# Kernel optimization log

Measured on AMD Instinct MI355X. Metric: run time of the kernel, lower is better.

## Reference

```python
import jax, jax.numpy as jnp
import numpy as np

B, T, S = 2, 1024, 1024
D_Q, D_KV, D_OUT = 2048, 2048, 2048
N_Q, N_KV, H = 16, 4, 128
G = N_Q // N_KV  # GQA groups
MIN_TS, MAX_TS = 1.0, 10000.0
SDPA_SCALE = 1.0  # dia uses scale=1.0 in F.scaled_dot_product_attention


def setup_inputs() -> dict:
    key = jax.random.key(0)
    ks = jax.random.split(key, 6)
    Xq = jax.random.normal(ks[0], (B, T, D_Q), jnp.float32)
    Xkv = jax.random.normal(ks[1], (B, S, D_KV), jnp.float32)
    q_positions = jnp.broadcast_to(jnp.arange(T, dtype=jnp.int32), (B, T))
    kv_positions = jnp.broadcast_to(jnp.arange(S, dtype=jnp.int32), (B, S))
    Wq = jax.random.normal(ks[2], (D_Q, N_Q, H), jnp.float32) * (D_Q ** -0.5)
    Wk = jax.random.normal(ks[3], (D_KV, N_KV, H), jnp.float32) * (D_KV ** -0.5)
    Wv = jax.random.normal(ks[4], (D_KV, N_KV, H), jnp.float32) * (D_KV ** -0.5)
    Wo = jax.random.normal(ks[5], (N_Q, H, D_OUT), jnp.float32) * ((N_Q * H) ** -0.5)
    return {"Xq": Xq, "Xkv": Xkv, "q_positions": q_positions,
            "kv_positions": kv_positions, "Wq": Wq, "Wk": Wk, "Wv": Wv, "Wo": Wo}


def _apply_rope(x, positions):
    # x: (B, L, N, H); positions: (B, L) int
    half = H // 2
    fraction = 2.0 * jnp.arange(half, dtype=jnp.float32) / H
    timescale = MIN_TS * (MAX_TS / MIN_TS) ** fraction  # (half,)
    sinusoid = positions.astype(jnp.float32)[:, :, None, None] / timescale  # (B,L,1,half)
    sin, cos = jnp.sin(sinusoid), jnp.cos(sinusoid)
    x = x.astype(jnp.float32)
    x1, x2 = jnp.split(x, 2, axis=-1)
    return jnp.concatenate([x1 * cos - x2 * sin, x2 * cos + x1 * sin], axis=-1)


def reference(Xq, Xkv, q_positions, kv_positions, Wq, Wk, Wv, Wo):
    # QKV projections (DenseGeneral): (B,L,D) x (D,N,H) -> (B,L,N,H)
    q = jnp.einsum('btd,dnh->btnh', Xq, Wq)
    k = jnp.einsum('bsd,dnh->bsnh', Xkv, Wk)
    v = jnp.einsum('bsd,dnh->bsnh', Xkv, Wv)
    # RoPE on q and k
    q = _apply_rope(q, q_positions)
    k = _apply_rope(k, kv_positions)
    # GQA attention, scale = 1.0 (as in dia), no mask, non-causal
    q = q.transpose(0, 2, 1, 3).reshape(B, N_KV, G, T, H)  # (B,K,G,T,H)
    k = k.transpose(0, 2, 1, 3)                             # (B,K,S,H)
    v = v.transpose(0, 2, 1, 3)                             # (B,K,S,H)
    scores = jnp.einsum('bkgth,bksh->bkgts', q, k) * SDPA_SCALE
    probs = jax.nn.softmax(scores, axis=-1)
    attn = jnp.einsum('bkgts,bksh->bkgth', probs, v)        # (B,K,G,T,H)
    attn = attn.reshape(B, N_Q, T, H).transpose(0, 2, 1, 3)  # (B,T,N,H)
    # Output projection (DenseGeneral contracting (N,H))
    out = jnp.einsum('btnh,nho->bto', attn, Wo)
    return out
```

## Files before the change

kernel.cpp:

```cpp
#include <hip/hip_runtime.h>
#include <hip/hip_bf16.h>
#include <math.h>
#include <stdint.h>

#define B_SZ 2
#define T_SZ 1024
#define S_SZ 1024
#define NQ 16
#define NKV 4
#define HD 128
#define DQ 2048
#define DKV 2048
#define DOUT 2048

typedef _Float16 half8 __attribute__((ext_vector_type(8)));
typedef _Float16 half4 __attribute__((ext_vector_type(4)));
typedef float f32x4 __attribute__((ext_vector_type(4)));

__device__ __forceinline__ half8 load8_f16(const _Float16* p) {
    return *reinterpret_cast<const half8*>(p);
}

__device__ __forceinline__ void stage16(const _Float16* g, _Float16* l, int lane) {
#if __has_builtin(__builtin_amdgcn_global_load_lds)
    __builtin_amdgcn_global_load_lds(
        (const __attribute__((address_space(1))) uint32_t*)g,
        (__attribute__((address_space(3))) uint32_t*)l, 16, 0, 0);
#else
    *reinterpret_cast<half8*>(l + lane * 8) = *reinterpret_cast<const half8*>(g);
#endif
}

__device__ __forceinline__ void conv_blk(const float* __restrict__ in,
                                         _Float16* __restrict__ out, int vb) {
    size_t i = ((size_t)vb * 256 + threadIdx.x) * 8;
    float4 a = *reinterpret_cast<const float4*>(in + i);
    float4 b = *reinterpret_cast<const float4*>(in + i + 4);
    half8 r;
    r[0] = (_Float16)a.x; r[1] = (_Float16)a.y; r[2] = (_Float16)a.z; r[3] = (_Float16)a.w;
    r[4] = (_Float16)b.x; r[5] = (_Float16)b.y; r[6] = (_Float16)b.z; r[7] = (_Float16)b.w;
    *reinterpret_cast<half8*>(out + i) = r;
}

__device__ __forceinline__ void tr_blk(const float* __restrict__ in,
                                       _Float16* __restrict__ out,
                                       int R, int C, int bx, int by,
                                       _Float16 (*tile)[72]) {
    const int tx = threadIdx.x & 15, ty = threadIdx.x >> 4;
    const int r0 = by * 64, c0 = bx * 64;
    #pragma unroll
    for (int i = 0; i < 4; ++i) {
        int r = ty + i * 16;
        float4 v = *reinterpret_cast<const float4*>(&in[(size_t)(r0 + r) * C + c0 + tx * 4]);
        tile[r][tx * 4 + 0] = (_Float16)v.x;
        tile[r][tx * 4 + 1] = (_Float16)v.y;
        tile[r][tx * 4 + 2] = (_Float16)v.z;
        tile[r][tx * 4 + 3] = (_Float16)v.w;
    }
    __syncthreads();
    #pragma unroll
    for (int i = 0; i < 4; ++i) {
        int oc = ty + i * 16;
        half4 v;
        v[0] = tile[tx * 4 + 0][oc];
        v[1] = tile[tx * 4 + 1][oc];
        v[2] = tile[tx * 4 + 2][oc];
        v[3] = tile[tx * 4 + 3][oc];
        *reinterpret_cast<half4*>(&out[(size_t)(c0 + oc) * R + r0 + tx * 4]) = v;
    }
}

__device__ __forceinline__ void tr16_blk(const _Float16* __restrict__ in,
                                         _Float16* __restrict__ out,
                                         int Cin, int Cout, int r0, int c0,
                                         _Float16 (*tile)[72]) {
    const int tx = threadIdx.x & 15, ty = threadIdx.x >> 4;
    #pragma unroll
    for (int i = 0; i < 4; ++i) {
        int r = ty + i * 16;
        half4 v = *reinterpret_cast<const half4*>(&in[(size_t)(r0 + r) * Cin + c0 + tx * 4]);
        tile[r][tx * 4 + 0] = v[0];
        tile[r][tx * 4 + 1] = v[1];
        tile[r][tx * 4 + 2] = v[2];
        tile[r][tx * 4 + 3] = v[3];
    }
    __syncthreads();
    #pragma unroll
    for (int i = 0; i < 4; ++i) {
        int oc = ty + i * 16;
        half4 v;
        v[0] = tile[tx * 4 + 0][oc];
        v[1] = tile[tx * 4 + 1][oc];
        v[2] = tile[tx * 4 + 2][oc];
        v[3] = tile[tx * 4 + 3][oc];
        *reinterpret_cast<half4*>(&out[(size_t)(c0 + oc) * Cout + r0 + tx * 4]) = v;
    }
}

__device__ __forceinline__ void rope_blk(_Float16* __restrict__ x,
                                         const int* __restrict__ pos,
                                         int N, int rowStride, int vb) {
    size_t idx = (size_t)vb * 256 + threadIdx.x;
    int h = (int)(idx & 63);
    size_t g = idx >> 6;
    int n = (int)(g % (size_t)N);
    size_t bl = g / (size_t)N;
    float p = (float)pos[bl];
    float ts = powf(10000.f, (float)h * (1.f / 64.f));
    float ang = p / ts;
    float s = sinf(ang), c = cosf(ang);
    size_t base = bl * (size_t)rowStride + (size_t)n * HD;
    float x1 = (float)x[base + h];
    float x2 = (float)x[base + h + 64];
    x[base + h]      = (_Float16)(x1 * c - x2 * s);
    x[base + h + 64] = (_Float16)(x2 * c + x1 * s);
}

__global__ __launch_bounds__(256) void prep1(const float* __restrict__ Xq, _Float16* __restrict__ Xq16,
                                             const float* __restrict__ Xkv, _Float16* __restrict__ Xkv16,
                                             const float* __restrict__ Wq, _Float16* __restrict__ WqT,
                                             const float* __restrict__ Wk, const float* __restrict__ Wv,
                                             _Float16* __restrict__ WkvT) {
    __shared__ _Float16 tile[64][72];
    int bx = blockIdx.x;
    if (bx < 2048) { conv_blk(Xq, Xq16, bx); return; }
    bx -= 2048;
    if (bx < 2048) { conv_blk(Xkv, Xkv16, bx); return; }
    bx -= 2048;
    if (bx < 1024) { tr_blk(Wq, WqT, 2048, 2048, bx & 31, bx >> 5, tile); return; }
    bx -= 1024;
    if (bx < 256) { tr_blk(Wk, WkvT, 2048, 512, bx & 7, bx >> 3, tile); return; }
    bx -= 256;
    tr_blk(Wv, WkvT + (size_t)512 * 2048, 2048, 512, bx & 7, bx >> 3, tile);
}

__global__ __launch_bounds__(256) void prep2(const float* __restrict__ Wo, _Float16* __restrict__ WoT,
                                             _Float16* __restrict__ Qh, const int* __restrict__ qpos,
                                             _Float16* __restrict__ KVh, const int* __restrict__ kpos,
                                             _Float16* __restrict__ VTh) {
    __shared__ _Float16 tile[64][72];
    int bx = blockIdx.x;
    if (bx < 1024) { tr_blk(Wo, WoT, 2048, 2048, bx & 31, bx >> 5, tile); return; }
    bx -= 1024;
    if (bx < 8192) { rope_blk(Qh, qpos, NQ, NQ * HD, bx); return; }
    bx -= 8192;
    if (bx < 2048) { rope_blk(KVh, kpos, NKV, 1024, bx); return; }
    bx -= 2048;
    {
        const int head = bx >> 5;
        const int t = bx & 31;
        const int sx = t & 15, hx = t >> 4;
        const int b = head >> 2, kn = head & 3;
        const _Float16* in = KVh + (size_t)(b * S_SZ) * 1024 + 512 + kn * HD;
        _Float16* out = VTh + (size_t)head * HD * S_SZ;
        tr16_blk(in, out, 1024, 1024, sx * 64, hx * 64, tile);
    }
}

template <int BM, int BN, typename TC>
__device__ __forceinline__ void gemm_tile(const _Float16* __restrict__ A,
                                          const _Float16* __restrict__ Bt,
                                          TC* __restrict__ C,
                                          int N, int K, int kbeg, int kend,
                                          int bm, int bn, _Float16* lds) {
    constexpr int ASEG = BM / 8, BSEG = BN / 8, TSEG = ASEG + BSEG, PSEG = TSEG / 4;
    constexpr int BUFSZ = TSEG * 512;
    const int tid = threadIdx.x, lane = tid & 63, w = tid >> 6;
    const int quad = lane >> 4, l16 = lane & 15;
    constexpr int WM = BM / 2, WN = BN / 2, MI = WM / 16, NI = WN / 16;
    const int wm = (w >> 1) * WM, wn = (w & 1) * WN;

    const int srl = lane >> 3;
    const int skb = (lane & 7) ^ srl;

    const _Float16* gp[PSEG];
    _Float16* lp[PSEG];
    #pragma unroll
    for (int p = 0; p < PSEG; ++p) {
        int s = w + p * 4;
        if (s < ASEG) {
            gp[p] = A + (size_t)(bm + s * 8 + srl) * K + kbeg + skb * 8;
        } else {
            gp[p] = Bt + (size_t)(bn + (s - ASEG) * 8 + srl) * K + kbeg + skb * 8;
        }
        lp[p] = lds + s * 512;
    }

    f32x4 acc[MI][NI];
    #pragma unroll
    for (int i = 0; i < MI; ++i)
        #pragma unroll
        for (int j = 0; j < NI; ++j)
            acc[i][j] = (f32x4){0.f, 0.f, 0.f, 0.f};

    const int nsteps = (kend - kbeg) >> 6;

    #pragma unroll
    for (int p = 0; p < PSEG; ++p)
        stage16(gp[p], lp[p], lane);
    __syncthreads();

    const int rxa = l16 & 7;
    int cur = 0;
    for (int it = 0; it < nsteps; ++it) {
        if (it + 1 < nsteps) {
            const int ko = (it + 1) * 64;
            const int nb = (cur ^ 1) * BUFSZ;
            #pragma unroll
            for (int p = 0; p < PSEG; ++p)
                stage16(gp[p] + ko, lp[p] + nb, lane);
        }
        const _Float16* lb = lds + cur * BUFSZ;
        #pragma unroll
        for (int h = 0; h < 2; ++h) {
            const int kb0 = h * 4 + quad;
            const int kswz = (kb0 ^ rxa) * 8;
            half8 af[MI], bf[NI];
            #pragma unroll
            for (int i = 0; i < MI; ++i) {
                const int r = wm + 16 * i + l16;
                af[i] = *reinterpret_cast<const half8*>(&lb[r * 64 + kswz]);
            }
            #pragma unroll
            for (int j = 0; j < NI; ++j) {
                const int r = wn + 16 * j + l16;
                bf[j] = *reinterpret_cast<const half8*>(&lb[BM * 64 + r * 64 + kswz]);
            }
            #pragma unroll
            for (int i = 0; i < MI; ++i)
                #pragma unroll
                for (int j = 0; j < NI; ++j)
                    acc[i][j] = __builtin_amdgcn_mfma_f32_16x16x32_f16(af[i], bf[j], acc[i][j], 0, 0, 0);
        }
        __syncthreads();
        cur ^= 1;
    }

    #pragma unroll
    for (int i = 0; i < MI; ++i)
        #pragma unroll
        for (int j = 0; j < NI; ++j)
            #pragma unroll
            for (int r = 0; r < 4; ++r) {
                size_t idx = (size_t)(bm + wm + 16 * i + quad * 4 + r) * N + bn + wn + 16 * j + l16;
                C[idx] = (TC)acc[i][j][r];
            }
}

__global__ __launch_bounds__(256) void proj_fused(const _Float16* __restrict__ Xq,
                                                  const _Float16* __restrict__ WqT,
                                                  _Float16* __restrict__ Qh,
                                                  const _Float16* __restrict__ Xkv,
                                                  const _Float16* __restrict__ WkvT,
                                                  _Float16* __restrict__ KVh) {
    __shared__ __align__(16) _Float16 lds[2 * (128 + 64) * 64];
    int bx = blockIdx.x;
    if (bx < 512) {
        gemm_tile<128, 64, _Float16>(Xq, WqT, Qh, 2048, 2048, 0, 2048,
                                     (bx & 15) * 128, (bx >> 4) * 64, lds);
    } else {
        bx -= 512;
        gemm_tile<128, 64, _Float16>(Xkv, WkvT, KVh, 1024, 2048, 0, 2048,
                                     (bx & 15) * 128, (bx >> 4) * 64, lds);
    }
}

__global__ __launch_bounds__(256) void gemm_out(const _Float16* __restrict__ A,
                                                const _Float16* __restrict__ Bt,
                                                float* __restrict__ C) {
    __shared__ __align__(16) _Float16 lds[2 * (128 + 64) * 64];
    const int bx = blockIdx.x;
    gemm_tile<128, 64, float>(A, Bt, C, 2048, 2048, 0, 2048,
                              (bx & 15) * 128, (bx >> 4) * 64, lds);
}

__global__ __launch_bounds__(256) void attn_kernel(const _Float16* __restrict__ Q,
                                                   const _Float16* __restrict__ KV,
                                                   const _Float16* __restrict__ VT,
                                                   _Float16* __restrict__ O) {
    __shared__ __align__(16) _Float16 Ks[64][136];
    __shared__ __align__(16) _Float16 Vt[128][72];
    __shared__ __align__(16) _Float16 Ps[4][16][72];
    const int tid = threadIdx.x, lane = tid & 63, w = tid >> 6;
    const int quad = lane >> 4, l16 = lane & 15;
    const int blk = blockIdx.x;
    const int t0 = (blk & 15) * 64;
    const int n  = (blk >> 4) & 15;
    const int b  = blk >> 8;
    const int kn = n >> 2;
    const _Float16* Vhead = VT + (size_t)(b * NKV + kn) * HD * S_SZ;

    half8 qf[4];
    #pragma unroll
    for (int kh = 0; kh < 4; ++kh)
        qf[kh] = load8_f16(&Q[(((size_t)b * T_SZ + t0 + w * 16 + l16) * NQ + n) * HD + kh * 32 + quad * 8]);

    f32x4 o_acc[8];
    #pragma unroll
    for (int i = 0; i < 8; ++i) o_acc[i] = (f32x4){0.f, 0.f, 0.f, 0.f};
    float m_row[4] = {-1e30f, -1e30f, -1e30f, -1e30f};
    float l_part[4] = {0.f, 0.f, 0.f, 0.f};

    for (int s0 = 0; s0 < S_SZ; s0 += 64) {
        __syncthreads();
        #pragma unroll
        for (int i = 0; i < 4; ++i) {
            int e = tid + i * 256;
            int r = e >> 4, c = (e & 15) * 8;
            *reinterpret_cast<half8*>(&Ks[r][c]) =
                load8_f16(&KV[(size_t)(b * S_SZ + s0 + r) * 1024 + kn * HD + c]);
            int vh = e >> 3, vc = (e & 7) * 8;
            *reinterpret_cast<half8*>(&Vt[vh][vc]) =
                load8_f16(&Vhead[(size_t)vh * S_SZ + s0 + vc]);
        }
        __syncthreads();

        f32x4 sf[4];
        __builtin_amdgcn_s_setprio(1);
        #pragma unroll
        for (int i4 = 0; i4 < 4; ++i4) {
            const int sc = i4 >> 1, j2 = i4 & 1;
            f32x4 sa = (f32x4){0.f, 0.f, 0.f, 0.f};
            #pragma unroll
            for (int kh = 0; kh < 4; ++kh) {
                half8 bk = *reinterpret_cast<const half8*>(
                    &Ks[sc * 32 + j2 * 16 + l16][kh * 32 + quad * 8]);
                sa = __builtin_amdgcn_mfma_f32_16x16x32_f16(qf[kh], bk, sa, 0, 0, 0);
            }
            sf[i4] = sa;
        }
        __builtin_amdgcn_s_setprio(0);
        #pragma unroll
        for (int r = 0; r < 4; ++r) {
            float mc = fmaxf(fmaxf(sf[0][r], sf[1][r]), fmaxf(sf[2][r], sf[3][r]));
            #pragma unroll
            for (int off = 1; off < 16; off <<= 1)
                mc = fmaxf(mc, __shfl_xor(mc, off, 64));
            float mn = fmaxf(m_row[r], mc);
            float alpha = __expf(m_row[r] - mn);
            m_row[r] = mn;
            float p0 = __expf(sf[0][r] - mn);
            float p1 = __expf(sf[1][r] - mn);
            float p2 = __expf(sf[2][r] - mn);
            float p3 = __expf(sf[3][r] - mn);
            l_part[r] = l_part[r] * alpha + (p0 + p1) + (p2 + p3);
            #pragma unroll
            for (int ht = 0; ht < 8; ++ht)
                o_acc[ht][r] *= alpha;
            Ps[w][quad * 4 + r][l16]      = (_Float16)p0;
            Ps[w][quad * 4 + r][16 + l16] = (_Float16)p1;
            Ps[w][quad * 4 + r][32 + l16] = (_Float16)p2;
            Ps[w][quad * 4 + r][48 + l16] = (_Float16)p3;
        }
        __builtin_amdgcn_wave_barrier();
        half8 ap0 = *reinterpret_cast<const half8*>(&Ps[w][l16][quad * 8]);
        half8 ap1 = *reinterpret_cast<const half8*>(&Ps[w][l16][32 + quad * 8]);
        __builtin_amdgcn_wave_barrier();
        __builtin_amdgcn_s_setprio(1);
        #pragma unroll
        for (int ht = 0; ht < 8; ++ht) {
            half8 bv0 = *reinterpret_cast<const half8*>(&Vt[ht * 16 + l16][quad * 8]);
            o_acc[ht] = __builtin_amdgcn_mfma_f32_16x16x32_f16(ap0, bv0, o_acc[ht], 0, 0, 0);
        }
        #pragma unroll
        for (int ht = 0; ht < 8; ++ht) {
            half8 bv1 = *reinterpret_cast<const half8*>(&Vt[ht * 16 + l16][32 + quad * 8]);
            o_acc[ht] = __builtin_amdgcn_mfma_f32_16x16x32_f16(ap1, bv1, o_acc[ht], 0, 0, 0);
        }
        __builtin_amdgcn_s_setprio(0);
    }

    float inv_l[4];
    #pragma unroll
    for (int r = 0; r < 4; ++r) {
        float l = l_part[r];
        #pragma unroll
        for (int off = 1; off < 16; off <<= 1)
            l += __shfl_xor(l, off, 64);
        inv_l[r] = 1.f / fmaxf(l, 1e-30f);
    }
    #pragma unroll
    for (int ht = 0; ht < 8; ++ht)
        #pragma unroll
        for (int r = 0; r < 4; ++r)
            O[(((size_t)b * T_SZ + t0 + w * 16 + quad * 4 + r) * NQ + n) * HD + ht * 16 + l16] =
                (_Float16)(o_acc[ht][r] * inv_l[r]);
}

extern "C" void kernel_launch(void* const* d_in, const int* in_sizes, int n_in,
                              void* d_out, int out_size, void* d_ws, size_t ws_size,
                              hipStream_t stream) {
    const float* Xq   = (const float*)d_in[0];
    const float* Xkv  = (const float*)d_in[1];
    const int*   qpos = (const int*)d_in[2];
    const int*   kpos = (const int*)d_in[3];
    const float* Wq   = (const float*)d_in[4];
    const float* Wk   = (const float*)d_in[5];
    const float* Wv   = (const float*)d_in[6];
    const float* Wo   = (const float*)d_in[7];
    float* out = (float*)d_out;

    const size_t SZ8 = 8388608;
    uint8_t* ws = (uint8_t*)d_ws;
    _Float16* Xq16  = (_Float16*)(ws);
    _Float16* Xkv16 = (_Float16*)(ws + SZ8);
    _Float16* WqT   = (_Float16*)(ws + 2 * SZ8);
    _Float16* WkvT  = (_Float16*)(ws + 3 * SZ8);
    _Float16* Qh    = (_Float16*)(ws + 3 * SZ8 + 4194304);
    _Float16* Ah  = Xq16;
    _Float16* WoT = Xkv16;
    _Float16* KVh = WqT;
    _Float16* VTh = WkvT;

    dim3 blk(256);
    prep1<<<5632, blk, 0, stream>>>(Xq, Xq16, Xkv, Xkv16, Wq, WqT, Wk, Wv, WkvT);
    proj_fused<<<768, blk, 0, stream>>>(Xq16, WqT, Qh, Xkv16, WkvT, KVh);
    prep2<<<11520, blk, 0, stream>>>(Wo, WoT, Qh, qpos, KVh, kpos, VTh);
    attn_kernel<<<512, blk, 0, stream>>>(Qh, KVh, VTh, Ah);
    gemm_out<<<512, blk, 0, stream>>>(Ah, WoT, out);
}
```

Baseline: 237.0 us.

## Double-buffer K/V tiles with async LDS loads, XOR swizzle, and lazy rescale

The attention kernel now stages K and V tiles into two alternating LDS buffers using the stage16 direct global-to-LDS helper. The next tile's load is issued before the current tile is computed, so memory latency can overlap with MFMA work, and padding is replaced by an XOR swizzle to avoid bank conflicts. The online-softmax rescale of the accumulators is skipped whenever no row max grew in the wave. The cost is doubled LDS use, which may lower occupancy, plus a wave-uniform branch.

```diff
diff --git a/kernel.cpp b/kernel.cpp
--- a/kernel.cpp
+++ b/kernel.cpp
@@ -278,8 +278,10 @@
                                                    const _Float16* __restrict__ KV,
                                                    const _Float16* __restrict__ VT,
                                                    _Float16* __restrict__ O) {
-    __shared__ __align__(16) _Float16 Ks[64][136];
-    __shared__ __align__(16) _Float16 Vt[128][72];
+    constexpr int KBUF = 64 * 128;
+    constexpr int VBUF = 128 * 64;
+    constexpr int BUFSZ = KBUF + VBUF;
+    __shared__ __align__(16) _Float16 lds[2 * BUFSZ];
     __shared__ __align__(16) _Float16 Ps[4][16][72];
     const int tid = threadIdx.x, lane = tid & 63, w = tid >> 6;
     const int quad = lane >> 4, l16 = lane & 15;
@@ -288,7 +290,13 @@
     const int n  = (blk >> 4) & 15;
     const int b  = blk >> 8;
     const int kn = n >> 2;
+    const _Float16* KVb  = KV + (size_t)b * S_SZ * 1024 + kn * HD;
     const _Float16* Vhead = VT + (size_t)(b * NKV + kn) * HD * S_SZ;
+
+    const int krow_i = lane >> 4;
+    const int kcp    = lane & 15;
+    const int vrow_i = lane >> 3;
+    const int vcp    = lane & 7;
 
     half8 qf[4];
     #pragma unroll
@@ -301,52 +309,83 @@
     float m_row[4] = {-1e30f, -1e30f, -1e30f, -1e30f};
     float l_part[4] = {0.f, 0.f, 0.f, 0.f};
 
-    for (int s0 = 0; s0 < S_SZ; s0 += 64) {
-        __syncthreads();
-        #pragma unroll
-        for (int i = 0; i < 4; ++i) {
-            int e = tid + i * 256;
-            int r = e >> 4, c = (e & 15) * 8;
-            *reinterpret_cast<half8*>(&Ks[r][c]) =
-                load8_f16(&KV[(size_t)(b * S_SZ + s0 + r) * 1024 + kn * HD + c]);
-            int vh = e >> 3, vc = (e & 7) * 8;
-            *reinterpret_cast<half8*>(&Vt[vh][vc]) =
-                load8_f16(&Vhead[(size_t)vh * S_SZ + s0 + vc]);
-        }
-        __syncthreads();
+    auto stage_tile = [&](int s0, int buf) {
+        _Float16* kb = lds + buf * BUFSZ;
+        _Float16* vb = kb + KBUF;
+        #pragma unroll
+        for (int j = 0; j < 4; ++j) {
+            const int s = w + j * 4;
+            const int row = 4 * s + krow_i;
+            const int kc = kcp ^ (row & 7);
+            stage16(KVb + (size_t)(s0 + row) * 1024 + kc * 8, kb + s * 512, lane);
+        }
+        #pragma unroll
+        for (int j = 0; j < 4; ++j) {
+            const int s = w + j * 4;
+            const int row = 8 * s + vrow_i;
+            const int vc = vcp ^ (row & 7);
+            stage16(Vhead + (size_t)row * S_SZ + s0 + vc * 8, vb + s * 512, lane);
+        }
+    };
+
+    stage_tile(0, 0);
+    __syncthreads();
+
+    const int rx = l16 & 7;
+    int cur = 0;
+    for (int t = 0; t < S_SZ / 64; ++t) {
+        if (t + 1 < S_SZ / 64)
+            stage_tile((t + 1) * 64, cur ^ 1);
+        const _Float16* Kb = lds + cur * BUFSZ;
+        const _Float16* Vb = Kb + KBUF;
 
         f32x4 sf[4];
         __builtin_amdgcn_s_setprio(1);
         #pragma unroll
         for (int i4 = 0; i4 < 4; ++i4) {
-            const int sc = i4 >> 1, j2 = i4 & 1;
+            const int srow = i4 * 16 + l16;
             f32x4 sa = (f32x4){0.f, 0.f, 0.f, 0.f};
             #pragma unroll
             for (int kh = 0; kh < 4; ++kh) {
+                const int c = kh * 4 + quad;
                 half8 bk = *reinterpret_cast<const half8*>(
-                    &Ks[sc * 32 + j2 * 16 + l16][kh * 32 + quad * 8]);
+                    &Kb[srow * 128 + ((c ^ rx) * 8)]);
                 sa = __builtin_amdgcn_mfma_f32_16x16x32_f16(qf[kh], bk, sa, 0, 0, 0);
             }
             sf[i4] = sa;
         }
         __builtin_amdgcn_s_setprio(0);
+
+        float mc[4];
         #pragma unroll
         for (int r = 0; r < 4; ++r) {
-            float mc = fmaxf(fmaxf(sf[0][r], sf[1][r]), fmaxf(sf[2][r], sf[3][r]));
+            float m0 = fmaxf(fmaxf(sf[0][r], sf[1][r]), fmaxf(sf[2][r], sf[3][r]));
             #pragma unroll
             for (int off = 1; off < 16; off <<= 1)
-                mc = fmaxf(mc, __shfl_xor(mc, off, 64));
-            float mn = fmaxf(m_row[r], mc);
-            float alpha = __expf(m_row[r] - mn);
-            m_row[r] = mn;
-            float p0 = __expf(sf[0][r] - mn);
-            float p1 = __expf(sf[1][r] - mn);
-            float p2 = __expf(sf[2][r] - mn);
-            float p3 = __expf(sf[3][r] - mn);
-            l_part[r] = l_part[r] * alpha + (p0 + p1) + (p2 + p3);
-            #pragma unroll
-            for (int ht = 0; ht < 8; ++ht)
-                o_acc[ht][r] *= alpha;
+                m0 = fmaxf(m0, __shfl_xor(m0, off, 64));
+            mc[r] = m0;
+        }
+        bool grow = (mc[0] > m_row[0]) | (mc[1] > m_row[1]) |
+                    (mc[2] > m_row[2]) | (mc[3] > m_row[3]);
+        if (__any(grow)) {
+            #pragma unroll
+            for (int r = 0; r < 4; ++r) {
+                float mn = fmaxf(m_row[r], mc[r]);
+                float alpha = __expf(m_row[r] - mn);
+                m_row[r] = mn;
+                l_part[r] *= alpha;
+                #pragma unroll
+                for (int ht = 0; ht < 8; ++ht)
+                    o_acc[ht][r] *= alpha;
+            }
+        }
+        #pragma unroll
+        for (int r = 0; r < 4; ++r) {
+            float p0 = __expf(sf[0][r] - m_row[r]);
+            float p1 = __expf(sf[1][r] - m_row[r]);
+            float p2 = __expf(sf[2][r] - m_row[r]);
+            float p3 = __expf(sf[3][r] - m_row[r]);
+            l_part[r] += (p0 + p1) + (p2 + p3);
             Ps[w][quad * 4 + r][l16]      = (_Float16)p0;
             Ps[w][quad * 4 + r][16 + l16] = (_Float16)p1;
             Ps[w][quad * 4 + r][32 + l16] = (_Float16)p2;
@@ -359,15 +398,18 @@
         __builtin_amdgcn_s_setprio(1);
         #pragma unroll
         for (int ht = 0; ht < 8; ++ht) {
-            half8 bv0 = *reinterpret_cast<const half8*>(&Vt[ht * 16 + l16][quad * 8]);
+            const int vrow = ht * 16 + l16;
+            half8 bv0 = *reinterpret_cast<const half8*>(
+                &Vb[vrow * 64 + ((quad ^ rx) * 8)]);
             o_acc[ht] = __builtin_amdgcn_mfma_f32_16x16x32_f16(ap0, bv0, o_acc[ht], 0, 0, 0);
-        }
-        #pragma unroll
-        for (int ht = 0; ht < 8; ++ht) {
-            half8 bv1 = *reinterpret_cast<const half8*>(&Vt[ht * 16 + l16][32 + quad * 8]);
+            half8 bv1 = *reinterpret_cast<const half8*>(
+                &Vb[vrow * 64 + (((4 + quad) ^ rx) * 8)]);
             o_acc[ht] = __builtin_amdgcn_mfma_f32_16x16x32_f16(ap1, bv1, o_acc[ht], 0, 0, 0);
         }
         __builtin_amdgcn_s_setprio(0);
+
+        __syncthreads();
+        cur ^= 1;
     }
 
     float inv_l[4];
```

Measured after the change: 233.0 us. Within noise of the previous version (-1.6%).
